# Kernel tuning notes

Measured on AMD Instinct MI355X. Metric: run time of the kernel, lower is better.

The kernel has to match this reference:

```python
import jax, jax.numpy as jnp
import numpy as np

NUM_HEADS = 8
HEAD_DIM = 64
INPUT_DIM = 512
OUT_DIM = 512
INNER_DIM = NUM_HEADS * HEAD_DIM


def setup_inputs() -> dict:
    key = jax.random.key(0)
    ks = jax.random.split(key, 5)
    B, T = 4, 2048
    x = jax.random.normal(ks[0], (B, T, INPUT_DIM), dtype=jnp.float32)
    Wk = jax.random.normal(ks[1], (INNER_DIM, INPUT_DIM), dtype=jnp.float32)
    Wq = jax.random.normal(ks[2], (INNER_DIM, INPUT_DIM), dtype=jnp.float32)
    Wv = jax.random.normal(ks[3], (INNER_DIM, INPUT_DIM), dtype=jnp.float32)
    Wp = jax.random.normal(ks[4], (OUT_DIM, INNER_DIM), dtype=jnp.float32)
    return {"x": x, "Wk": Wk, "Wq": Wq, "Wv": Wv, "Wp": Wp, "causal_mask": 0}


def reference(x, Wk, Wq, Wv, Wp, causal_mask):
    B, T, C = x.shape
    c_scale = C ** (-0.5)

    def proj(W):
        # (B,T,C) @ (C,inner) -> (B,T,H,D) -> (B,H,T,D), scaled by C^-0.5
        return (jnp.einsum('btc,ic->bti', x, W)
                .reshape(B, T, NUM_HEADS, HEAD_DIM)
                .transpose(0, 2, 1, 3) * c_scale)

    q, k, v = proj(Wq), proj(Wk), proj(Wv)
    # scores: (B,H,T,T), scaled by head_dim^-0.5
    weight = jnp.einsum('bhqd,bhkd->bhqk', q, k) * (HEAD_DIM ** (-0.5))
    if causal_mask:
        mask = jnp.triu(jnp.ones((T, T), dtype=bool), k=1)
        weight = jnp.where(mask, -jnp.inf, weight)
    weight = jax.nn.softmax(weight, axis=-1)
    out = jnp.einsum('bhqk,bhkd->bhqd', weight, v)  # (B,H,T,D)
    out = out.transpose(0, 2, 1, 3).reshape(B, T, INNER_DIM)
    # final projection scaled by inner_dim^-0.5 (projection.size(-1))
    out = jnp.einsum('bti,oi->bto', out, Wp) * (INNER_DIM ** (-0.5))
    return out
```

## Files before the change

kernel.cpp:

```cpp
#include <hip/hip_runtime.h>
#include <stdint.h>

#define T_SEQ 2048
#define NB 4
#define NH 8
#define DH 64
#define CD 512

typedef __attribute__((ext_vector_type(8))) short bf16x8;
typedef __attribute__((ext_vector_type(4))) uint16_t u16x4;
typedef __attribute__((ext_vector_type(4))) float f32x4;
typedef __attribute__((ext_vector_type(16))) float f32x16;
typedef __attribute__((ext_vector_type(4))) int i32x4;

#if __has_builtin(__builtin_amdgcn_exp2f)
#define EXP2(x) __builtin_amdgcn_exp2f(x)
#else
#define EXP2(x) exp2f(x)
#endif

__device__ __forceinline__ uint16_t f2bf(float f) {
  uint32_t u = __float_as_uint(f);
  u += 0x7FFFu + ((u >> 16) & 1u);
  return (uint16_t)(u >> 16);
}

__device__ __forceinline__ uint32_t cvtpk_bf16(float lo, float hi) {
  uint32_t r;
  asm("v_cvt_pk_bf16_f32 %0, %1, %2" : "=v"(r) : "v"(lo), "v"(hi));
  return r;
}

__device__ __forceinline__ void gload_lds16(const void* g, void* l) {
  __builtin_amdgcn_global_load_lds((const __attribute__((address_space(1))) void*)g,
                                   (__attribute__((address_space(3))) void*)l, 16, 0, 0);
}

__global__ __launch_bounds__(256) void cvt_all(const float* __restrict__ x,
    const float* __restrict__ wq, const float* __restrict__ wk,
    const float* __restrict__ wv, const float* __restrict__ wp,
    uint16_t* __restrict__ ws) {
  int i = blockIdx.x * 256 + threadIdx.x;
  int e = i * 4;
  const float* src;
  uint16_t* dst;
  if (e < 4194304) {
    src = x + e; dst = ws + e;
  } else {
    int r = e - 4194304;
    int w = r >> 18;
    int o = r & 262143;
    const float* W = (w == 0) ? wq : (w == 1) ? wk : (w == 2) ? wv : wp;
    src = W + o;
    dst = ws + 4194304 + (w << 18) + o;
  }
  float4 v = *(const float4*)src;
  u16x4 o4 = { f2bf(v.x), f2bf(v.y), f2bf(v.z), f2bf(v.w) };
  *(u16x4*)dst = o4;
}

__device__ __forceinline__ void gemm_bt_tile(const uint16_t* __restrict__ A,
                                             const uint16_t* __restrict__ Bt,
                                             int m0, int n0,
                                             uint16_t* As, uint16_t* Bs,
                                             f32x4 acc[4][4]) {
  const int tid = threadIdx.x;
  const int lane = tid & 63;
  const int wave = tid >> 6;
  const int wr = (wave >> 1) * 64, wc = (wave & 1) * 64;
  const int l15 = lane & 15, l4 = lane >> 4;

#pragma unroll
  for (int m = 0; m < 4; ++m)
#pragma unroll
    for (int n = 0; n < 4; ++n)
      acc[m][n] = (f32x4){0.f, 0.f, 0.f, 0.f};

  for (int kt = 0; kt < 8; ++kt) {
#pragma unroll
    for (int is = 0; is < 4; ++is) {
      int p = is * 4096 + tid * 16;
      int g = p ^ (((p >> 7) & 7) << 4);
      int row = g >> 7, colb = g & 127;
      gload_lds16((const char*)A + (size_t)(m0 + row) * 1024 + kt * 128 + colb,
                  (char*)As + p);
      gload_lds16((const char*)Bt + (size_t)(n0 + row) * 1024 + kt * 128 + colb,
                  (char*)Bs + p);
    }
    __syncthreads();
#pragma unroll
    for (int ks = 0; ks < 2; ++ks) {
      bf16x8 af[4], bfr[4];
#pragma unroll
      for (int m = 0; m < 4; ++m) {
        int row = wr + m * 16 + l15;
        int byt = (row * 128 + ks * 64 + l4 * 16) ^ ((row & 7) << 4);
        af[m] = *(const bf16x8*)((const char*)As + byt);
      }
#pragma unroll
      for (int n = 0; n < 4; ++n) {
        int row = wc + n * 16 + l15;
        int byt = (row * 128 + ks * 64 + l4 * 16) ^ ((row & 7) << 4);
        bfr[n] = *(const bf16x8*)((const char*)Bs + byt);
      }
#pragma unroll
      for (int m = 0; m < 4; ++m)
#pragma unroll
        for (int n = 0; n < 4; ++n)
          acc[m][n] = __builtin_amdgcn_mfma_f32_16x16x32_bf16(af[m], bfr[n], acc[m][n], 0, 0, 0);
    }
    __syncthreads();
  }
}

__global__ __launch_bounds__(256) void proj_kernel(const uint16_t* __restrict__ xb,
    const uint16_t* __restrict__ wbase, uint16_t* __restrict__ qkv,
    float qscale, float kvscale) {
  __shared__ __align__(16) uint16_t As[128 * 64];
  __shared__ __align__(16) uint16_t Bs[128 * 64];
  int z = blockIdx.z;
  const uint16_t* W = wbase + (size_t)z * 262144;
  uint16_t* outb = qkv + (size_t)z * 4194304;
  float scale = (z == 0) ? qscale : kvscale;
  f32x4 acc[4][4];
  int lane = threadIdx.x & 63, wave = threadIdx.x >> 6;
  int wr = (wave >> 1) * 64, wc = (wave & 1) * 64;
  int l15 = lane & 15, l4 = lane >> 4;

  if (z < 2) {
    int m0 = blockIdx.x * 128, n0 = blockIdx.y * 128;
    gemm_bt_tile(xb, W, m0, n0, As, Bs, acc);
#pragma unroll
    for (int m = 0; m < 4; ++m)
#pragma unroll
      for (int n = 0; n < 4; ++n)
#pragma unroll
        for (int j = 0; j < 4; ++j) {
          int row = m0 + wr + m * 16 + l4 * 4 + j;
          int col = n0 + wc + n * 16 + l15;
          int b = row >> 11, t = row & 2047;
          int h = col >> 6, d = col & 63;
          outb[((size_t)(b * NH + h) * T_SEQ + t) * DH + d] = f2bf(acc[m][n][j] * scale);
        }
  } else {
    int m0 = blockIdx.y * 128, n0 = blockIdx.x * 128;
    gemm_bt_tile(W, xb, m0, n0, As, Bs, acc);
#pragma unroll
    for (int m = 0; m < 4; ++m)
#pragma unroll
      for (int n = 0; n < 4; ++n)
#pragma unroll
        for (int j = 0; j < 4; ++j) {
          int row = m0 + wr + m * 16 + l4 * 4 + j;
          int col = n0 + wc + n * 16 + l15;
          int h = row >> 6, d = row & 63;
          int b = col >> 11, t = col & 2047;
          outb[((size_t)(b * NH + h) * DH + d) * T_SEQ + t] = f2bf(acc[m][n][j] * scale);
        }
  }
}

__global__ __launch_bounds__(256) void attn2(const uint16_t* __restrict__ Q,
    const uint16_t* __restrict__ K, const uint16_t* __restrict__ VT,
    uint16_t* __restrict__ AO) {
  __shared__ __align__(16) uint16_t Ka[2][4096];
  __shared__ __align__(16) uint16_t Va[2][4096];

  int bid = blockIdx.x;
  int swz = (bid & 7) * 64 + (bid >> 3);
  int qt = swz & 15, bh = swz >> 4;
  int b = bh >> 3, h = bh & 7;
  int tid = threadIdx.x, lane = tid & 63, wave = tid >> 6;
  int l31 = lane & 31, hi = lane >> 5;

  const uint16_t* Kb  = K  + (size_t)bh * T_SEQ * DH;
  const uint16_t* VTb = VT + (size_t)bh * DH * T_SEQ;
  const uint16_t* Qrow = Q + ((size_t)bh * T_SEQ + qt * 128 + wave * 32 + l31) * DH;

  bf16x8 qf[4];
#pragma unroll
  for (int m = 0; m < 4; ++m)
    qf[m] = *(const bf16x8*)((const char*)Qrow + m * 32 + hi * 16);

  f32x16 Oacc[2];
#pragma unroll
  for (int dB = 0; dB < 2; ++dB) Oacc[dB] = (f32x16)(0.f);
  float lpart = 0.f;

  {
#pragma unroll
    for (int c = 0; c < 2; ++c) {
      int p = c * 4096 + tid * 16;
      int g = p ^ (((p >> 7) & 7) << 4);
      gload_lds16((const char*)Kb + g, (char*)(&Ka[0][0]) + p);
      int row = g >> 7, off = g & 127;
      gload_lds16((const char*)VTb + (size_t)row * 4096 + off, (char*)(&Va[0][0]) + p);
    }
  }
  __syncthreads();

  for (int kt = 0; kt < 32; ++kt) {
    const char* Kc = (const char*)(&Ka[kt & 1][0]);
    const char* Vc = (const char*)(&Va[kt & 1][0]);

    if (kt + 1 < 32) {
      int nb = (kt + 1) & 1;
      const char* ksrc = (const char*)Kb + (size_t)(kt + 1) * 8192;
#pragma unroll
      for (int c = 0; c < 2; ++c) {
        int p = c * 4096 + tid * 16;
        int g = p ^ (((p >> 7) & 7) << 4);
        gload_lds16(ksrc + g, (char*)(&Ka[nb][0]) + p);
        int row = g >> 7, off = g & 127;
        gload_lds16((const char*)VTb + (size_t)row * 4096 + (size_t)(kt + 1) * 128 + off,
                    (char*)(&Va[nb][0]) + p);
      }
    }

    f32x16 s0 = (f32x16)(0.f), s1 = (f32x16)(0.f);
#pragma unroll
    for (int m = 0; m < 4; ++m) {
      int row0 = l31;
      int byt0 = (row0 * 128 + m * 32 + hi * 16) ^ ((row0 & 7) << 4);
      bf16x8 kf0 = *(const bf16x8*)(Kc + byt0);
      s0 = __builtin_amdgcn_mfma_f32_32x32x16_bf16(kf0, qf[m], s0, 0, 0, 0);
      int row1 = 32 + l31;
      int byt1 = (row1 * 128 + m * 32 + hi * 16) ^ ((row1 & 7) << 4);
      bf16x8 kf1 = *(const bf16x8*)(Kc + byt1);
      s1 = __builtin_amdgcn_mfma_f32_32x32x16_bf16(kf1, qf[m], s1, 0, 0, 0);
    }

    uint32_t pa_[2][4], pb_[2][4];
    {
      float e0[16], e1[16];
#pragma unroll
      for (int r = 0; r < 16; ++r) { e0[r] = EXP2(s0[r]); lpart += e0[r]; }
#pragma unroll
      for (int r = 0; r < 16; ++r) { e1[r] = EXP2(s1[r]); lpart += e1[r]; }
#pragma unroll
      for (int g = 0; g < 4; ++g) {
        pa_[0][g] = cvtpk_bf16(e0[4 * g], e0[4 * g + 1]);
        pb_[0][g] = cvtpk_bf16(e0[4 * g + 2], e0[4 * g + 3]);
        pa_[1][g] = cvtpk_bf16(e1[4 * g], e1[4 * g + 1]);
        pb_[1][g] = cvtpk_bf16(e1[4 * g + 2], e1[4 * g + 3]);
      }
    }

#pragma unroll
    for (int km = 0; km < 4; ++km) {
      const int Tt = km >> 1;
      const int g0 = (km & 1) * 2;
      uint32_t aA = pa_[Tt][g0], aB = pa_[Tt][g0 + 1];
      uint32_t bA = pb_[Tt][g0], bB = pb_[Tt][g0 + 1];
      uint32_t aAx = (uint32_t)__shfl_xor((int)aA, 32, 64);
      uint32_t aBx = (uint32_t)__shfl_xor((int)aB, 32, 64);
      uint32_t bAx = (uint32_t)__shfl_xor((int)bA, 32, 64);
      uint32_t bBx = (uint32_t)__shfl_xor((int)bB, 32, 64);
      uint32_t w0 = hi ? aBx : aA;
      uint32_t w1 = hi ? bBx : bA;
      uint32_t w2 = hi ? aB : aAx;
      uint32_t w3 = hi ? bB : bAx;
      i32x4 pw = { (int)w0, (int)w1, (int)w2, (int)w3 };
      bf16x8 paf = __builtin_bit_cast(bf16x8, pw);
#pragma unroll
      for (int dB = 0; dB < 2; ++dB) {
        int row = dB * 32 + l31;
        int byt = (row * 128 + km * 32 + hi * 16) ^ ((row & 7) << 4);
        bf16x8 vf = *(const bf16x8*)(Vc + byt);
        Oacc[dB] = __builtin_amdgcn_mfma_f32_32x32x16_bf16(paf, vf, Oacc[dB], 0, 0, 0);
      }
    }

    __syncthreads();
  }

  float lsum = lpart + __shfl_xor(lpart, 32, 64);
  float inv = 1.f / lsum;
  int qb0 = qt * 128 + wave * 32;
#pragma unroll
  for (int r = 0; r < 16; ++r) {
    int qoff = (r & 3) + 8 * (r >> 2) + 4 * hi;
    float invr = __shfl(inv, qoff, 64);
    int t = qb0 + qoff;
    size_t base = ((size_t)(b * T_SEQ + t)) * 512 + h * 64;
    AO[base + l31]      = f2bf(Oacc[0][r] * invr);
    AO[base + 32 + l31] = f2bf(Oacc[1][r] * invr);
  }
}

__global__ __launch_bounds__(256) void final_kernel(const uint16_t* __restrict__ ab,
    const uint16_t* __restrict__ wpb, float* __restrict__ out, float scale) {
  __shared__ __align__(16) uint16_t As[128 * 64];
  __shared__ __align__(16) uint16_t Bs[128 * 64];
  int m0 = blockIdx.x * 128, n0 = blockIdx.y * 128;
  f32x4 acc[4][4];
  gemm_bt_tile(ab, wpb, m0, n0, As, Bs, acc);
  int lane = threadIdx.x & 63, wave = threadIdx.x >> 6;
  int wr = (wave >> 1) * 64, wc = (wave & 1) * 64;
  int l15 = lane & 15, l4 = lane >> 4;
#pragma unroll
  for (int m = 0; m < 4; ++m)
#pragma unroll
    for (int n = 0; n < 4; ++n)
#pragma unroll
      for (int j = 0; j < 4; ++j) {
        int row = m0 + wr + m * 16 + l4 * 4 + j;
        int col = n0 + wc + n * 16 + l15;
        out[(size_t)row * 512 + col] = acc[m][n][j] * scale;
      }
}

extern "C" void kernel_launch(void* const* d_in, const int* in_sizes, int n_in,
                              void* d_out, int out_size, void* d_ws, size_t ws_size,
                              hipStream_t stream) {
  const float* x  = (const float*)d_in[0];
  const float* Wk = (const float*)d_in[1];
  const float* Wq = (const float*)d_in[2];
  const float* Wv = (const float*)d_in[3];
  const float* Wp = (const float*)d_in[4];
  uint16_t* ws = (uint16_t*)d_ws;

  uint16_t* xb  = ws;
  uint16_t* wqb = ws + 4194304;
  uint16_t* qkv = ws + 4194304 + 4 * 262144;
  uint16_t* qb  = qkv;
  uint16_t* kb  = qkv + 4194304;
  uint16_t* vtb = qkv + 2 * 4194304;
  uint16_t* ao  = xb;
  uint16_t* wpb = wqb + 3 * 262144;

  const float c_scale = 0.04419417382415922f;
  const float qscale = c_scale * 0.125f * 1.4426950408889634f;
  const float fscale = c_scale;

  cvt_all<<<dim3(5120), dim3(256), 0, stream>>>(x, Wq, Wk, Wv, Wp, ws);
  proj_kernel<<<dim3(64, 4, 3), dim3(256), 0, stream>>>(xb, wqb, qkv, qscale, c_scale);
  attn2<<<dim3(512), dim3(256), 0, stream>>>(qb, kb, vtb, ao);
  final_kernel<<<dim3(64, 4), dim3(256), 0, stream>>>(ao, wpb, (float*)d_out, fscale);
}
```

Before: 101.7 us.

## Deepen attention K/V prefetch to 4 LDS buffers with single vmcnt barrier

The attention kernel now cycles through four LDS buffers, prefetching two tiles ahead. A manual s_waitcnt vmcnt plus one s_barrier per iteration replaces the two __syncthreads calls. The P-fragment exchange between lane halves uses v_permlane32_swap instead of four shuffles and selects, and s_setprio is raised around the MFMA blocks. The row-sum accumulation is split into four partial sums to shorten the dependency chain. LDS use doubles to 64KB per block, which may reduce occupancy, and the hand-written waitcnt counts must match the number of loads issued.

```diff
diff --git a/kernel.cpp b/kernel.cpp
--- a/kernel.cpp
+++ b/kernel.cpp
@@ -160,11 +160,11 @@
   }
 }
 
-__global__ __launch_bounds__(256) void attn2(const uint16_t* __restrict__ Q,
+__global__ __launch_bounds__(256) void attn3(const uint16_t* __restrict__ Q,
     const uint16_t* __restrict__ K, const uint16_t* __restrict__ VT,
     uint16_t* __restrict__ AO) {
-  __shared__ __align__(16) uint16_t Ka[2][4096];
-  __shared__ __align__(16) uint16_t Va[2][4096];
+  __shared__ __align__(16) uint16_t Ka[4][4096];
+  __shared__ __align__(16) uint16_t Va[4][4096];
 
   int bid = blockIdx.x;
   int swz = (bid & 7) * 64 + (bid >> 3);
@@ -177,47 +177,45 @@
   const uint16_t* VTb = VT + (size_t)bh * DH * T_SEQ;
   const uint16_t* Qrow = Q + ((size_t)bh * T_SEQ + qt * 128 + wave * 32 + l31) * DH;
 
-  bf16x8 qf[4];
-#pragma unroll
-  for (int m = 0; m < 4; ++m)
-    qf[m] = *(const bf16x8*)((const char*)Qrow + m * 32 + hi * 16);
-
-  f32x16 Oacc[2];
-#pragma unroll
-  for (int dB = 0; dB < 2; ++dB) Oacc[dB] = (f32x16)(0.f);
-  float lpart = 0.f;
-
-  {
+  auto stage = [&](int t) {
+    int bufi = t & 3;
+    const char* ksrc = (const char*)Kb + (size_t)t * 8192;
 #pragma unroll
     for (int c = 0; c < 2; ++c) {
       int p = c * 4096 + tid * 16;
       int g = p ^ (((p >> 7) & 7) << 4);
-      gload_lds16((const char*)Kb + g, (char*)(&Ka[0][0]) + p);
+      gload_lds16(ksrc + g, (char*)(&Ka[bufi][0]) + p);
       int row = g >> 7, off = g & 127;
-      gload_lds16((const char*)VTb + (size_t)row * 4096 + off, (char*)(&Va[0][0]) + p);
-    }
-  }
-  __syncthreads();
+      gload_lds16((const char*)VTb + (size_t)row * 4096 + (size_t)t * 128 + off,
+                  (char*)(&Va[bufi][0]) + p);
+    }
+  };
+
+  bf16x8 qf[4];
+#pragma unroll
+  for (int m = 0; m < 4; ++m)
+    qf[m] = *(const bf16x8*)((const char*)Qrow + m * 32 + hi * 16);
+
+  f32x16 Oacc[2];
+#pragma unroll
+  for (int dB = 0; dB < 2; ++dB) Oacc[dB] = (f32x16)(0.f);
+  float lp0 = 0.f, lp1 = 0.f, lp2 = 0.f, lp3 = 0.f;
+
+  stage(0);
+  stage(1);
 
   for (int kt = 0; kt < 32; ++kt) {
-    const char* Kc = (const char*)(&Ka[kt & 1][0]);
-    const char* Vc = (const char*)(&Va[kt & 1][0]);
-
-    if (kt + 1 < 32) {
-      int nb = (kt + 1) & 1;
-      const char* ksrc = (const char*)Kb + (size_t)(kt + 1) * 8192;
-#pragma unroll
-      for (int c = 0; c < 2; ++c) {
-        int p = c * 4096 + tid * 16;
-        int g = p ^ (((p >> 7) & 7) << 4);
-        gload_lds16(ksrc + g, (char*)(&Ka[nb][0]) + p);
-        int row = g >> 7, off = g & 127;
-        gload_lds16((const char*)VTb + (size_t)row * 4096 + (size_t)(kt + 1) * 128 + off,
-                    (char*)(&Va[nb][0]) + p);
-      }
-    }
+    if (kt + 2 < 32) stage(kt + 2);
+
+    if (kt < 30)       asm volatile("s_waitcnt vmcnt(8)\n\ts_barrier" ::: "memory");
+    else if (kt == 30) asm volatile("s_waitcnt vmcnt(4)\n\ts_barrier" ::: "memory");
+    else               asm volatile("s_waitcnt vmcnt(0)\n\ts_barrier" ::: "memory");
+
+    const char* Kc = (const char*)(&Ka[kt & 3][0]);
+    const char* Vc = (const char*)(&Va[kt & 3][0]);
 
     f32x16 s0 = (f32x16)(0.f), s1 = (f32x16)(0.f);
+    __builtin_amdgcn_s_setprio(1);
 #pragma unroll
     for (int m = 0; m < 4; ++m) {
       int row0 = l31;
@@ -229,14 +227,22 @@
       bf16x8 kf1 = *(const bf16x8*)(Kc + byt1);
       s1 = __builtin_amdgcn_mfma_f32_32x32x16_bf16(kf1, qf[m], s1, 0, 0, 0);
     }
+    __builtin_amdgcn_s_setprio(0);
 
     uint32_t pa_[2][4], pb_[2][4];
     {
       float e0[16], e1[16];
 #pragma unroll
-      for (int r = 0; r < 16; ++r) { e0[r] = EXP2(s0[r]); lpart += e0[r]; }
-#pragma unroll
-      for (int r = 0; r < 16; ++r) { e1[r] = EXP2(s1[r]); lpart += e1[r]; }
+      for (int r = 0; r < 16; ++r) e0[r] = EXP2(s0[r]);
+#pragma unroll
+      for (int r = 0; r < 16; ++r) e1[r] = EXP2(s1[r]);
+#pragma unroll
+      for (int r = 0; r < 16; ++r) {
+        if ((r & 3) == 0)      { lp0 += e0[r]; lp0 += e1[r]; }
+        else if ((r & 3) == 1) { lp1 += e0[r]; lp1 += e1[r]; }
+        else if ((r & 3) == 2) { lp2 += e0[r]; lp2 += e1[r]; }
+        else                   { lp3 += e0[r]; lp3 += e1[r]; }
+      }
 #pragma unroll
       for (int g = 0; g < 4; ++g) {
         pa_[0][g] = cvtpk_bf16(e0[4 * g], e0[4 * g + 1]);
@@ -250,18 +256,13 @@
     for (int km = 0; km < 4; ++km) {
       const int Tt = km >> 1;
       const int g0 = (km & 1) * 2;
-      uint32_t aA = pa_[Tt][g0], aB = pa_[Tt][g0 + 1];
-      uint32_t bA = pb_[Tt][g0], bB = pb_[Tt][g0 + 1];
-      uint32_t aAx = (uint32_t)__shfl_xor((int)aA, 32, 64);
-      uint32_t aBx = (uint32_t)__shfl_xor((int)aB, 32, 64);
-      uint32_t bAx = (uint32_t)__shfl_xor((int)bA, 32, 64);
-      uint32_t bBx = (uint32_t)__shfl_xor((int)bB, 32, 64);
-      uint32_t w0 = hi ? aBx : aA;
-      uint32_t w1 = hi ? bBx : bA;
-      uint32_t w2 = hi ? aB : aAx;
-      uint32_t w3 = hi ? bB : bAx;
+      uint32_t w0 = pa_[Tt][g0], w2 = pa_[Tt][g0 + 1];
+      uint32_t w1 = pb_[Tt][g0], w3 = pb_[Tt][g0 + 1];
+      asm volatile("v_permlane32_swap_b32 %0, %1" : "+v"(w0), "+v"(w2));
+      asm volatile("v_permlane32_swap_b32 %0, %1" : "+v"(w1), "+v"(w3));
       i32x4 pw = { (int)w0, (int)w1, (int)w2, (int)w3 };
       bf16x8 paf = __builtin_bit_cast(bf16x8, pw);
+      __builtin_amdgcn_s_setprio(1);
 #pragma unroll
       for (int dB = 0; dB < 2; ++dB) {
         int row = dB * 32 + l31;
@@ -269,11 +270,11 @@
         bf16x8 vf = *(const bf16x8*)(Vc + byt);
         Oacc[dB] = __builtin_amdgcn_mfma_f32_32x32x16_bf16(paf, vf, Oacc[dB], 0, 0, 0);
       }
-    }
-
-    __syncthreads();
-  }
-
+      __builtin_amdgcn_s_setprio(0);
+    }
+  }
+
+  float lpart = (lp0 + lp1) + (lp2 + lp3);
   float lsum = lpart + __shfl_xor(lpart, 32, 64);
   float inv = 1.f / lsum;
   int qb0 = qt * 128 + wave * 32;
@@ -335,6 +336,6 @@
 
   cvt_all<<<dim3(5120), dim3(256), 0, stream>>>(x, Wq, Wk, Wv, Wp, ws);
   proj_kernel<<<dim3(64, 4, 3), dim3(256), 0, stream>>>(xb, wqb, qkv, qscale, c_scale);
-  attn2<<<dim3(512), dim3(256), 0, stream>>>(qb, kb, vtb, ao);
+  attn3<<<dim3(512), dim3(256), 0, stream>>>(qb, kb, vtb, ao);
   final_kernel<<<dim3(64, 4), dim3(256), 0, stream>>>(ao, wpb, (float*)d_out, fscale);
 }
```

After: 98.94 us. -2.7%, faster.
